# Kernel tuning notes

Measured on AMD Instinct MI355X. Metric: run time of the kernel, lower is better.

Reference implementation:

```python
import jax, jax.numpy as jnp
import numpy as np

B, N, M, C1, C2 = 16, 4096, 1024, 128, 256
MLP0, MLP1 = 256, 256
IN_CH = C1 + C2
EPS = 1e-5


def setup_inputs() -> dict:
    key = jax.random.key(0)
    ks = jax.random.split(key, 6)
    return {
        "xyz1": jax.random.normal(ks[0], (B, 3, N), jnp.float32),
        "xyz2": jax.random.normal(ks[1], (B, 3, M), jnp.float32),
        "points1": jax.random.normal(ks[2], (B, C1, N), jnp.float32),
        "points2": jax.random.normal(ks[3], (B, C2, M), jnp.float32),
        "W1": jax.random.normal(ks[4], (MLP0, IN_CH), jnp.float32) * (1.0 / np.sqrt(IN_CH)),
        "gamma1": jnp.ones((MLP0,), jnp.float32),
        "beta1": jnp.zeros((MLP0,), jnp.float32),
        "W2": jax.random.normal(ks[5], (MLP1, MLP0), jnp.float32) * (1.0 / np.sqrt(MLP0)),
        "gamma2": jnp.ones((MLP1,), jnp.float32),
        "beta2": jnp.zeros((MLP1,), jnp.float32),
    }


def _batchnorm(x, gamma, beta):
    # x: (B, N, C); normalize per channel over batch*length (training-mode BN, biased var)
    mean = jnp.mean(x, axis=(0, 1))
    var = jnp.mean((x - mean) ** 2, axis=(0, 1))
    return (x - mean) * jax.lax.rsqrt(var + EPS) * gamma + beta


def reference(xyz1, xyz2, points1, points2, W1, gamma1, beta1, W2, gamma2, beta2):
    p1 = jnp.swapaxes(xyz1, 1, 2)  # (B, N, 3)
    p2 = jnp.swapaxes(xyz2, 1, 2)  # (B, M, 3)
    # squared pairwise distances (B, N, M); squaring preserves 3-NN ordering,
    # and the original squares the euclidean dist before weighting anyway
    d2 = jnp.sum((p1[:, :, None, :] - p2[:, None, :, :]) ** 2, axis=-1)
    neg_d2, idx = jax.lax.top_k(-d2, 3)  # 3 smallest distances
    dist2 = jnp.maximum(-neg_d2, 1e-10)  # (B, N, 3)
    inv = 1.0 / dist2
    weight = inv / jnp.sum(inv, axis=-1, keepdims=True)  # (B, N, 3)
    f2 = jnp.swapaxes(points2, 1, 2)  # (B, M, C2)
    b, n, k = idx.shape
    gathered = jnp.take_along_axis(
        f2, idx.reshape(b, n * k)[:, :, None], axis=1
    ).reshape(b, n, k, -1)  # (B, N, 3, C2)
    interp = jnp.einsum("bnk,bnkc->bnc", weight, gathered)  # (B, N, C2)
    feat = jnp.concatenate([interp, jnp.swapaxes(points1, 1, 2)], axis=-1)  # (B, N, C1+C2)
    h = jnp.einsum("bnc,oc->bno", feat, W1)  # conv1d k=1, no bias
    h = jax.nn.relu(_batchnorm(h, gamma1, beta1))
    h = jnp.einsum("bnc,oc->bno", h, W2)
    h = jax.nn.relu(_batchnorm(h, gamma2, beta2))
    return jnp.swapaxes(h, 1, 2)  # (B, MLP1, N), channel-first like torch
```

## Files before the change

### kernel.cpp

```cpp
#include <hip/hip_runtime.h>

typedef unsigned short u16;
typedef unsigned int u32;

#define BB 16
#define NN 4096
#define MM 1024
#define C1V 128
#define C2V 256
#define EPSV 1e-5f
#define INV_CNT (1.0f/65536.0f)
#define NREP 32

typedef __attribute__((ext_vector_type(8))) short bf16x8;
typedef __attribute__((ext_vector_type(4))) float f32x4;

static __device__ __forceinline__ u16 f2b(float f) {
  u32 u = __float_as_uint(f);
  u32 r = (u + 0x7FFFu + ((u >> 16) & 1u)) >> 16;
  return (u16)r;
}
static __device__ __forceinline__ float b2f(u16 s) {
  return __uint_as_float(((u32)s) << 16);
}

#define GLD_LDS16(gp, lp)                                                      \
  __builtin_amdgcn_global_load_lds(                                            \
      (const __attribute__((address_space(1))) void*)(gp),                     \
      (__attribute__((address_space(3))) void*)(lp), 16, 0, 0)

__device__ __forceinline__ void tcast_tile64(const float* __restrict__ in,
                                             u16* __restrict__ out, int C,
                                             int P, int p0, int c0, int b,
                                             float (*tile)[33]) {
  int tx = threadIdx.x & 31, ty = threadIdx.x >> 5;
  const float* ib = in + (size_t)b * C * P;
  u16* ob = out + (size_t)b * P * C;
#pragma unroll
  for (int i = 0; i < 8; ++i)
    tile[ty + i * 8][tx] = ib[(size_t)(c0 + ty + i * 8) * P + p0 + tx];
  __syncthreads();
#pragma unroll
  for (int i = 0; i < 4; ++i) {
    int p = ty + i * 8;
    u32 v = (u32)f2b(tile[tx * 2][p]) | ((u32)f2b(tile[tx * 2 + 1][p]) << 16);
    *(u32*)&ob[(size_t)(p0 + p) * C + c0 + tx * 2] = v;
  }
}

__global__ __launch_bounds__(256) void prep_kernel(
    const float* __restrict__ xyz1, const float* __restrict__ xyz2,
    float* __restrict__ pd, int* __restrict__ pi,
    const float* __restrict__ points1, const float* __restrict__ points2,
    u16* __restrict__ p1t, u16* __restrict__ p2t,
    const float* __restrict__ W1, const float* __restrict__ W2,
    u16* __restrict__ W1b, u16* __restrict__ W2b,
    float* __restrict__ statsZero) {
  __shared__ float4 cand[256];
  __shared__ float tile[64][33];
  int bx = blockIdx.x;
  int t = threadIdx.x;

  if (bx < 1024) {
    int c = bx & 3;
    int qt = (bx >> 2) & 15;
    int b = bx >> 6;
    const float* x2b = xyz2 + b * 3 * MM;
    {
      float x = x2b[c * 256 + t];
      float y = x2b[MM + c * 256 + t];
      float z = x2b[2 * MM + c * 256 + t];
      cand[t] = make_float4(x, y, z, x * x + y * y + z * z);
    }
    __syncthreads();
    const float* x1b = xyz1 + b * 3 * NN;
    int n = qt * 256 + t;
    float px = x1b[n], py = x1b[NN + n], pz = x1b[2 * NN + n];
    const float INF = 3.4e38f;
    float k0 = INF, k1 = INF, k2 = INF;
    int j0 = 0, j1 = 0, j2 = 0;
#pragma unroll 8
    for (int m = 0; m < 256; ++m) {
      float4 cd = cand[m];
      float dot = fmaf(px, cd.x, fmaf(py, cd.y, pz * cd.z));
      float key = fmaf(-2.0f, dot, cd.w);
      bool c0 = key < k0, c1 = key < k1, c2 = key < k2;
      k2 = c1 ? k1 : (c2 ? key : k2);
      j2 = c1 ? j1 : (c2 ? m : j2);
      k1 = c0 ? k0 : (c1 ? key : k1);
      j1 = c0 ? j0 : (c1 ? m : j1);
      k0 = c0 ? key : k0;
      j0 = c0 ? m : j0;
    }
    float pn = px * px + py * py + pz * pz;
    int gq = b * NN + n;
    int base = c << 8;
    ((float4*)pd)[(size_t)c * 65536 + gq] =
        make_float4(fmaxf(k0 + pn, 1e-10f), fmaxf(k1 + pn, 1e-10f),
                    fmaxf(k2 + pn, 1e-10f), 0.0f);
    ((int4*)pi)[(size_t)c * 65536 + gq] =
        make_int4(base + j0, base + j1, base + j2, 0);
  } else if (bx < 1664) {
    int i = (bx - 1024) * 256 + t;
    if (i < 98304) W1b[i] = f2b(W1[i]);
    else if (i < 163840) W2b[i - 98304] = f2b(W2[i - 98304]);
  } else if (bx < 1696) {
    ((float4*)statsZero)[(bx - 1664) * 256 + t] =
        make_float4(0.f, 0.f, 0.f, 0.f);
  } else if (bx < 3744) {
    int local = bx - 1696;
    int pt = local & 31, ct = (local >> 5) & 3, b = local >> 7;
    tcast_tile64(points2, p2t, C2V, MM, pt * 32, ct * 64, b, tile);
  } else {
    int local = bx - 3744;
    int pt = local & 127, ct = (local >> 7) & 1, b = local >> 8;
    tcast_tile64(points1, p1t, C1V, NN, pt * 32, ct * 64, b, tile);
  }
}

template <int K, int NTILES, bool OUTB>
__global__ __launch_bounds__(256) void gemm_mfma(
    const u16* __restrict__ A, int lda, const u16* __restrict__ B, int ldb,
    void* __restrict__ out) {
  __shared__ u16 smem[16384];
  int t = threadIdx.x;
  int w = t >> 6, l = t & 63;
  int n0;
  if (NTILES > 0) {
    int p = blockIdx.x;
    int batch = ((p & 7) << 1) | ((p >> 3) & 1);
    int nt = p >> 4;
    n0 = (batch * NTILES + nt) * 128;
  } else {
    n0 = blockIdx.x * 128;
  }
  int o0 = blockIdx.y * 128;

  int wm = w & 1, wn = w >> 1;
  int lr = l >> 2, lc = l & 3;
  int q = l >> 4, m = l & 15;

  f32x4 acc[4][4] = {};
  u16* As = smem;
  u16* Bs = smem + 4096;

  const u16* arow = A + (size_t)n0 * lda;
  const u16* brow = B + (size_t)o0 * ldb;

#pragma unroll
  for (int kt = 0; kt < K; kt += 32) {
    __syncthreads();
#pragma unroll
    for (int r = 0; r < 2; ++r) {
      int row = r * 64 + w * 16 + lr;
      GLD_LDS16(arow + (size_t)row * lda + kt + lc * 8, As + row * 32 + lc * 8);
    }
#pragma unroll
    for (int r = 0; r < 2; ++r) {
      int row = r * 64 + w * 16 + lr;
      GLD_LDS16(brow + (size_t)row * ldb + kt + lc * 8, Bs + row * 32 + lc * 8);
    }
    __syncthreads();
    bf16x8 af[4], bf[4];
#pragma unroll
    for (int i = 0; i < 4; ++i)
      af[i] = *(const bf16x8*)(As + (wm * 64 + i * 16 + m) * 32 + q * 8);
#pragma unroll
    for (int j = 0; j < 4; ++j)
      bf[j] = *(const bf16x8*)(Bs + (wn * 64 + j * 16 + m) * 32 + q * 8);
#pragma unroll
    for (int i = 0; i < 4; ++i)
#pragma unroll
      for (int j = 0; j < 4; ++j)
        acc[i][j] =
            __builtin_amdgcn_mfma_f32_16x16x32_bf16(af[i], bf[j], acc[i][j], 0, 0, 0);
  }

  if (OUTB) {
    __syncthreads();
#pragma unroll
    for (int i = 0; i < 4; ++i)
#pragma unroll
      for (int reg = 0; reg < 4; ++reg) {
        int row = wm * 64 + i * 16 + q * 4 + reg;
#pragma unroll
        for (int j = 0; j < 4; ++j)
          smem[row * 128 + wn * 64 + j * 16 + m] = f2b(acc[i][j][reg]);
      }
    __syncthreads();
    u16* outp = (u16*)out;
    int rbase = w * 32 + (l >> 4);
    int seg = l & 15;
#pragma unroll
    for (int itr = 0; itr < 8; ++itr) {
      int row = rbase + itr * 4;
      uint4 v = *(const uint4*)(smem + row * 128 + seg * 8);
      *(uint4*)(outp + (size_t)(n0 + row) * 256 + o0 + seg * 8) = v;
    }
  } else {
#pragma unroll
    for (int i = 0; i < 4; ++i) {
      int gr = n0 + wm * 64 + i * 16 + q * 4;
#pragma unroll
      for (int reg = 0; reg < 4; ++reg)
#pragma unroll
        for (int j = 0; j < 4; ++j) {
          int gc = o0 + wn * 64 + j * 16 + m;
          ((float*)out)[(size_t)(gr + reg) * 256 + gc] = acc[i][j][reg];
        }
    }
  }
}

__global__ __launch_bounds__(256) void gemm1_32(
    const u16* __restrict__ A, const u16* __restrict__ B,
    u16* __restrict__ out, const u16* __restrict__ G,
    const float* __restrict__ pd, const int* __restrict__ pi,
    float* __restrict__ statsOut) {
  __shared__ __align__(16) u16 smem[9216];
  __shared__ float wsh[32][3];
  __shared__ int ish[32][3];
  int t = threadIdx.x;
  int w = t >> 6, l = t & 63;
  int p = blockIdx.x;
  int batch = ((p & 7) << 1) | ((p >> 3) & 1);
  int nt = p >> 4;
  int n0 = batch * NN + nt * 32;

  if (t < 32) {
    int gq = n0 + t;
    float4 d0 = ((const float4*)pd)[gq];
    int4 ii0 = ((const int4*)pi)[gq];
    float a0 = d0.x, a1 = d0.y, a2 = d0.z;
    int b0 = ii0.x, b1 = ii0.y, b2 = ii0.z;
#pragma unroll
    for (int c = 1; c < 4; ++c) {
      float4 dc = ((const float4*)pd)[(size_t)c * 65536 + gq];
      int4 ic = ((const int4*)pi)[(size_t)c * 65536 + gq];
      float kv[3] = {dc.x, dc.y, dc.z};
      int jv[3] = {ic.x, ic.y, ic.z};
#pragma unroll
      for (int j = 0; j < 3; ++j) {
        float key = kv[j];
        int idx = jv[j];
        bool c0 = key < a0, c1 = key < a1, c2 = key < a2;
        a2 = c1 ? a1 : (c2 ? key : a2);
        b2 = c1 ? b1 : (c2 ? idx : b2);
        a1 = c0 ? a0 : (c1 ? key : a1);
        b1 = c0 ? b0 : (c1 ? idx : b1);
        a0 = c0 ? key : a0;
        b0 = c0 ? idx : b0;
      }
    }
    float v0 = 1.0f / a0, v1 = 1.0f / a1, v2 = 1.0f / a2;
    float s = 1.0f / (v0 + v1 + v2);
    wsh[t][0] = v0 * s; wsh[t][1] = v1 * s; wsh[t][2] = v2 * s;
    ish[t][0] = b0;     ish[t][1] = b1;     ish[t][2] = b2;
  }

  int q = l >> 4, m = l & 15;
  int sr = l >> 2, lc = l & 3;

  f32x4 acc[2][4] = {};
  u16* As = smem;
  u16* Bs = smem + 1024;
  const u16* arow = A + (size_t)n0 * 128;

#pragma unroll
  for (int kt = 0; kt < 128; kt += 32) {
    __syncthreads();
    if (w < 2) {
      int row = w * 16 + sr;
      GLD_LDS16(arow + (size_t)row * 128 + kt + lc * 8, As + row * 32 + lc * 8);
    }
#pragma unroll
    for (int r = 0; r < 4; ++r) {
      int row = r * 64 + w * 16 + sr;
      GLD_LDS16(B + (size_t)row * 384 + kt + lc * 8, Bs + row * 32 + lc * 8);
    }
    __syncthreads();
    bf16x8 af[2], bf[4];
#pragma unroll
    for (int i = 0; i < 2; ++i)
      af[i] = *(const bf16x8*)(As + (i * 16 + m) * 32 + q * 8);
#pragma unroll
    for (int j = 0; j < 4; ++j)
      bf[j] = *(const bf16x8*)(Bs + (w * 64 + j * 16 + m) * 32 + q * 8);
#pragma unroll
    for (int i = 0; i < 2; ++i)
#pragma unroll
      for (int j = 0; j < 4; ++j)
        acc[i][j] =
            __builtin_amdgcn_mfma_f32_16x16x32_bf16(af[i], bf[j], acc[i][j], 0, 0, 0);
  }

  __syncthreads();
  {
    int b = n0 >> 12;
    int rl = t >> 3, oc = t & 7;
    float w0 = wsh[rl][0], w1 = wsh[rl][1], w2 = wsh[rl][2];
    const u16* g0 = G + ((size_t)(b * 1024 + ish[rl][0])) * 256 + oc * 32;
    const u16* g1 = G + ((size_t)(b * 1024 + ish[rl][1])) * 256 + oc * 32;
    const u16* g2 = G + ((size_t)(b * 1024 + ish[rl][2])) * 256 + oc * 32;
    int r3 = rl & 7;
#pragma unroll
    for (int c8 = 0; c8 < 4; ++c8) {
      bf16x8 v0 = *(const bf16x8*)(g0 + c8 * 8);
      bf16x8 v1 = *(const bf16x8*)(g1 + c8 * 8);
      bf16x8 v2 = *(const bf16x8*)(g2 + c8 * 8);
      union { uint4 u; u16 s[8]; } o;
#pragma unroll
      for (int e = 0; e < 8; ++e) {
        float f = w0 * b2f((u16)v0[e]) + w1 * b2f((u16)v1[e]) +
                  w2 * b2f((u16)v2[e]);
        o.s[e] = f2b(f);
      }
      int ch = (oc * 4 + c8) ^ r3;
      *(uint4*)(smem + rl * 256 + ch * 8) = o.u;
    }
  }
  __syncthreads();
#pragma unroll
  for (int i = 0; i < 2; ++i)
#pragma unroll
    for (int reg = 0; reg < 4; ++reg) {
      int row = i * 16 + q * 4 + reg;
      int rx = row & 7;
#pragma unroll
      for (int j = 0; j < 4; ++j) {
        int col = w * 64 + j * 16 + m;
        int off = row * 256 + (((col >> 3) ^ rx) << 3) + (col & 7);
        acc[i][j][reg] += b2f(smem[off]);
      }
    }

  {
    int rep = blockIdx.x & (NREP - 1);
#pragma unroll
    for (int j = 0; j < 4; ++j) {
      float s = 0.0f, ss = 0.0f;
#pragma unroll
      for (int i = 0; i < 2; ++i)
#pragma unroll
        for (int reg = 0; reg < 4; ++reg) {
          float v = acc[i][j][reg];
          s += v;
          ss += v * v;
        }
      s += __shfl_down(s, 32); ss += __shfl_down(ss, 32);
      s += __shfl_down(s, 16); ss += __shfl_down(ss, 16);
      if (l < 16) {
        int c = w * 64 + j * 16 + l;
        atomicAdd(&statsOut[rep * 512 + c], s);
        atomicAdd(&statsOut[rep * 512 + 256 + c], ss);
      }
    }
  }

  __syncthreads();
#pragma unroll
  for (int i = 0; i < 2; ++i)
#pragma unroll
    for (int reg = 0; reg < 4; ++reg) {
      int row = i * 16 + q * 4 + reg;
#pragma unroll
      for (int j = 0; j < 4; ++j)
        smem[row * 256 + w * 64 + j * 16 + m] = f2b(acc[i][j][reg]);
    }
  __syncthreads();
  int rbase = t >> 5, seg = t & 31;
#pragma unroll
  for (int itr = 0; itr < 4; ++itr) {
    int row = rbase + itr * 8;
    uint4 v = *(const uint4*)(smem + row * 256 + seg * 8);
    *(uint4*)(out + (size_t)(n0 + row) * 256 + seg * 8) = v;
  }
}

__global__ __launch_bounds__(256) void gemm2_32(
    const u16* __restrict__ A, const u16* __restrict__ B,
    u16* __restrict__ out, float* __restrict__ statsOut,
    const float* __restrict__ statsInR, const float* __restrict__ gamma,
    const float* __restrict__ beta) {
  __shared__ __align__(16) u16 smem[9216];
  __shared__ float scA[256], shA[256];
  int t = threadIdx.x;
  int w = t >> 6, l = t & 63;
  int n0 = blockIdx.x * 32;

  {
    float s = 0.0f, qq = 0.0f;
#pragma unroll
    for (int r = 0; r < NREP; ++r) {
      s += statsInR[r * 512 + t];
      qq += statsInR[r * 512 + 256 + t];
    }
    float mean = s * INV_CNT;
    float var = qq * INV_CNT - mean * mean;
    float sc = rsqrtf(var + EPSV) * gamma[t];
    scA[t] = sc;
    shA[t] = beta[t] - mean * sc;
  }

  int q = l >> 4, m = l & 15;
  int sr = l >> 2, lc = l & 3;

  f32x4 acc[2][4] = {};
  u16* As = smem;
  u16* Bs = smem + 1024;
  const u16* arow = A + (size_t)n0 * 256;

#pragma unroll
  for (int kt = 0; kt < 256; kt += 32) {
    __syncthreads();
    if (w < 2) {
      int row = w * 16 + sr;
      union { uint4 u; u16 s[8]; } v, o;
      v.u = *(const uint4*)(arow + (size_t)row * 256 + kt + lc * 8);
      int cb = kt + lc * 8;
#pragma unroll
      for (int j = 0; j < 8; ++j) {
        float f = fmaf(b2f(v.s[j]), scA[cb + j], shA[cb + j]);
        o.s[j] = f2b(fmaxf(f, 0.0f));
      }
      *(uint4*)(As + row * 32 + lc * 8) = o.u;
    }
#pragma unroll
    for (int r = 0; r < 4; ++r) {
      int row = r * 64 + w * 16 + sr;
      GLD_LDS16(B + (size_t)row * 256 + kt + lc * 8, Bs + row * 32 + lc * 8);
    }
    __syncthreads();
    bf16x8 af[2], bf[4];
#pragma unroll
    for (int i = 0; i < 2; ++i)
      af[i] = *(const bf16x8*)(As + (i * 16 + m) * 32 + q * 8);
#pragma unroll
    for (int j = 0; j < 4; ++j)
      bf[j] = *(const bf16x8*)(Bs + (w * 64 + j * 16 + m) * 32 + q * 8);
#pragma unroll
    for (int i = 0; i < 2; ++i)
#pragma unroll
      for (int j = 0; j < 4; ++j)
        acc[i][j] =
            __builtin_amdgcn_mfma_f32_16x16x32_bf16(af[i], bf[j], acc[i][j], 0, 0, 0);
  }

  {
    int rep = blockIdx.x & (NREP - 1);
#pragma unroll
    for (int j = 0; j < 4; ++j) {
      float s = 0.0f, ss = 0.0f;
#pragma unroll
      for (int i = 0; i < 2; ++i)
#pragma unroll
        for (int reg = 0; reg < 4; ++reg) {
          float v = acc[i][j][reg];
          s += v;
          ss += v * v;
        }
      s += __shfl_down(s, 32); ss += __shfl_down(ss, 32);
      s += __shfl_down(s, 16); ss += __shfl_down(ss, 16);
      if (l < 16) {
        int c = w * 64 + j * 16 + l;
        atomicAdd(&statsOut[rep * 512 + c], s);
        atomicAdd(&statsOut[rep * 512 + 256 + c], ss);
      }
    }
  }

  __syncthreads();
#pragma unroll
  for (int i = 0; i < 2; ++i)
#pragma unroll
    for (int reg = 0; reg < 4; ++reg) {
      int row = i * 16 + q * 4 + reg;
#pragma unroll
      for (int j = 0; j < 4; ++j)
        smem[row * 256 + w * 64 + j * 16 + m] = f2b(acc[i][j][reg]);
    }
  __syncthreads();
  int rbase = t >> 5, seg = t & 31;
#pragma unroll
  for (int itr = 0; itr < 4; ++itr) {
    int row = rbase + itr * 8;
    uint4 v = *(const uint4*)(smem + row * 256 + seg * 8);
    *(uint4*)(out + (size_t)(n0 + row) * 256 + seg * 8) = v;
  }
}

__global__ __launch_bounds__(256) void bn2t_kernel(
    const u16* __restrict__ h2, const float* __restrict__ statsR,
    const float* __restrict__ gamma, const float* __restrict__ beta,
    float* __restrict__ out) {
  __shared__ float tile[64][65];
  __shared__ float sS[64], sH[64];
  int t = threadIdx.x;
  int n0 = blockIdx.x * 64, c0 = blockIdx.y * 64, b = blockIdx.z;
  if (t < 64) {
    int c = c0 + t;
    float s = 0.0f, qq = 0.0f;
#pragma unroll
    for (int r = 0; r < NREP; ++r) {
      s += statsR[r * 512 + c];
      qq += statsR[r * 512 + 256 + c];
    }
    float mean = s * INV_CNT;
    float var = qq * INV_CNT - mean * mean;
    float sc = rsqrtf(var + EPSV) * gamma[c];
    sS[t] = sc;
    sH[t] = beta[c] - mean * sc;
  }
  __syncthreads();
  int tx = t & 15, ty = t >> 4;
#pragma unroll
  for (int i = 0; i < 4; ++i) {
    int n = ty + i * 16;
    uint2 v = *(const uint2*)(h2 + ((size_t)b * NN + n0 + n) * 256 + c0 + tx * 4);
    int c = tx * 4;
    tile[n][c + 0] = fmaxf(fmaf(b2f((u16)(v.x & 0xffff)), sS[c + 0], sH[c + 0]), 0.0f);
    tile[n][c + 1] = fmaxf(fmaf(b2f((u16)(v.x >> 16)),    sS[c + 1], sH[c + 1]), 0.0f);
    tile[n][c + 2] = fmaxf(fmaf(b2f((u16)(v.y & 0xffff)), sS[c + 2], sH[c + 2]), 0.0f);
    tile[n][c + 3] = fmaxf(fmaf(b2f((u16)(v.y >> 16)),    sS[c + 3], sH[c + 3]), 0.0f);
  }
  __syncthreads();
#pragma unroll
  for (int i = 0; i < 4; ++i) {
    int c = ty + i * 16;
    int nq = tx * 4;
    float4 o4 = make_float4(tile[nq + 0][c], tile[nq + 1][c],
                            tile[nq + 2][c], tile[nq + 3][c]);
    *(float4*)(out + ((size_t)(b * 256 + c0 + c)) * NN + n0 + nq) = o4;
  }
}

extern "C" void kernel_launch(void* const* d_in, const int* in_sizes, int n_in,
                              void* d_out, int out_size, void* d_ws,
                              size_t ws_size, hipStream_t stream) {
  const float* xyz1    = (const float*)d_in[0];
  const float* xyz2    = (const float*)d_in[1];
  const float* points1 = (const float*)d_in[2];
  const float* points2 = (const float*)d_in[3];
  const float* W1      = (const float*)d_in[4];
  const float* gamma1  = (const float*)d_in[5];
  const float* beta1   = (const float*)d_in[6];
  const float* W2      = (const float*)d_in[7];
  const float* gamma2  = (const float*)d_in[8];
  const float* beta2   = (const float*)d_in[9];

  char* ws = (char*)d_ws;
  float* stats1R = (float*)(ws + 0);
  float* stats2R = (float*)(ws + 65536);
  u16*   W1b     = (u16*)(ws + 131072);
  u16*   W2b     = (u16*)(ws + 327680);
  u16*   p2t     = (u16*)(ws + 458752);
  u16*   p1t     = (u16*)(ws + 8847360);
  u16*   G       = (u16*)(ws + 25624576);
  u16*   h2b     = (u16*)(ws + 34013184);
  float* pd      = (float*)(ws + 67567616);
  int*   pi      = (int*)(ws + 71761920);
  u16*   h1b     = (u16*)d_out;
  float* out     = (float*)d_out;

  prep_kernel<<<7840, 256, 0, stream>>>(xyz1, xyz2, pd, pi, points1, points2,
                                        p1t, p2t, W1, W2, W1b, W2b, stats1R);
  gemm_mfma<256, 8, true><<<dim3(128, 2), 256, 0, stream>>>(p2t, 256, W1b, 384,
                                                            G);
  gemm1_32<<<2048, 256, 0, stream>>>(p1t, W1b + 256, h1b, G, pd, pi, stats1R);
  gemm2_32<<<2048, 256, 0, stream>>>(h1b, W2b, h2b, stats2R, stats1R, gamma1,
                                     beta1);
  bn2t_kernel<<<dim3(64, 4, 16), 256, 0, stream>>>(h2b, stats2R, gamma2,
                                                   beta2, out);
}
```

Measured before the change: 222.7 us.

## Interpolate raw features inside GEMM1 instead of precomputing projected G; double-buffer GEMM2

The separate GEMM that projected points2 through the first 256 columns of W1 (G = p2t·W1a) is removed. GEMM1 now builds the interpolated 256-channel feature rows on the fly from p2t, using the 3-NN weights, and runs the full K=384 reduction per 64-row tile. GEMM2 moves to 64-row tiles with double-buffered LDS, so the next A/B slices load while the current MFMAs run. This saves one kernel launch and the G round-trip, but GEMM1 now does 3x more MFMA work and gathers along the K loop with unpipelined global loads.

```diff
diff --git a/kernel.cpp b/kernel.cpp
--- a/kernel.cpp
+++ b/kernel.cpp
@@ -118,116 +118,22 @@
   }
 }
 
-template <int K, int NTILES, bool OUTB>
-__global__ __launch_bounds__(256) void gemm_mfma(
-    const u16* __restrict__ A, int lda, const u16* __restrict__ B, int ldb,
-    void* __restrict__ out) {
-  __shared__ u16 smem[16384];
-  int t = threadIdx.x;
-  int w = t >> 6, l = t & 63;
-  int n0;
-  if (NTILES > 0) {
-    int p = blockIdx.x;
-    int batch = ((p & 7) << 1) | ((p >> 3) & 1);
-    int nt = p >> 4;
-    n0 = (batch * NTILES + nt) * 128;
-  } else {
-    n0 = blockIdx.x * 128;
-  }
-  int o0 = blockIdx.y * 128;
-
-  int wm = w & 1, wn = w >> 1;
-  int lr = l >> 2, lc = l & 3;
-  int q = l >> 4, m = l & 15;
-
-  f32x4 acc[4][4] = {};
-  u16* As = smem;
-  u16* Bs = smem + 4096;
-
-  const u16* arow = A + (size_t)n0 * lda;
-  const u16* brow = B + (size_t)o0 * ldb;
-
-#pragma unroll
-  for (int kt = 0; kt < K; kt += 32) {
-    __syncthreads();
-#pragma unroll
-    for (int r = 0; r < 2; ++r) {
-      int row = r * 64 + w * 16 + lr;
-      GLD_LDS16(arow + (size_t)row * lda + kt + lc * 8, As + row * 32 + lc * 8);
-    }
-#pragma unroll
-    for (int r = 0; r < 2; ++r) {
-      int row = r * 64 + w * 16 + lr;
-      GLD_LDS16(brow + (size_t)row * ldb + kt + lc * 8, Bs + row * 32 + lc * 8);
-    }
-    __syncthreads();
-    bf16x8 af[4], bf[4];
-#pragma unroll
-    for (int i = 0; i < 4; ++i)
-      af[i] = *(const bf16x8*)(As + (wm * 64 + i * 16 + m) * 32 + q * 8);
-#pragma unroll
-    for (int j = 0; j < 4; ++j)
-      bf[j] = *(const bf16x8*)(Bs + (wn * 64 + j * 16 + m) * 32 + q * 8);
-#pragma unroll
-    for (int i = 0; i < 4; ++i)
-#pragma unroll
-      for (int j = 0; j < 4; ++j)
-        acc[i][j] =
-            __builtin_amdgcn_mfma_f32_16x16x32_bf16(af[i], bf[j], acc[i][j], 0, 0, 0);
-  }
-
-  if (OUTB) {
-    __syncthreads();
-#pragma unroll
-    for (int i = 0; i < 4; ++i)
-#pragma unroll
-      for (int reg = 0; reg < 4; ++reg) {
-        int row = wm * 64 + i * 16 + q * 4 + reg;
-#pragma unroll
-        for (int j = 0; j < 4; ++j)
-          smem[row * 128 + wn * 64 + j * 16 + m] = f2b(acc[i][j][reg]);
-      }
-    __syncthreads();
-    u16* outp = (u16*)out;
-    int rbase = w * 32 + (l >> 4);
-    int seg = l & 15;
-#pragma unroll
-    for (int itr = 0; itr < 8; ++itr) {
-      int row = rbase + itr * 4;
-      uint4 v = *(const uint4*)(smem + row * 128 + seg * 8);
-      *(uint4*)(outp + (size_t)(n0 + row) * 256 + o0 + seg * 8) = v;
-    }
-  } else {
-#pragma unroll
-    for (int i = 0; i < 4; ++i) {
-      int gr = n0 + wm * 64 + i * 16 + q * 4;
-#pragma unroll
-      for (int reg = 0; reg < 4; ++reg)
-#pragma unroll
-        for (int j = 0; j < 4; ++j) {
-          int gc = o0 + wn * 64 + j * 16 + m;
-          ((float*)out)[(size_t)(gr + reg) * 256 + gc] = acc[i][j][reg];
-        }
-    }
-  }
-}
-
-__global__ __launch_bounds__(256) void gemm1_32(
-    const u16* __restrict__ A, const u16* __restrict__ B,
-    u16* __restrict__ out, const u16* __restrict__ G,
+__global__ __launch_bounds__(256) void gemm1f(
+    const u16* __restrict__ p1t, const u16* __restrict__ W1b,
+    u16* __restrict__ out, const u16* __restrict__ p2t,
     const float* __restrict__ pd, const int* __restrict__ pi,
     float* __restrict__ statsOut) {
-  __shared__ __align__(16) u16 smem[9216];
-  __shared__ float wsh[32][3];
-  __shared__ int ish[32][3];
+  __shared__ __align__(16) u16 smem[16384];
+  __shared__ float wsh[64][3];
+  __shared__ int ish[64][3];
   int t = threadIdx.x;
   int w = t >> 6, l = t & 63;
   int p = blockIdx.x;
   int batch = ((p & 7) << 1) | ((p >> 3) & 1);
   int nt = p >> 4;
-  int n0 = batch * NN + nt * 32;
-
-  if (t < 32) {
+  int n0 = batch * NN + nt * 64;
+
+  if (t < 64) {
     int gq = n0 + t;
     float4 d0 = ((const float4*)pd)[gq];
     int4 ii0 = ((const int4*)pi)[gq];
@@ -257,90 +163,72 @@
     wsh[t][0] = v0 * s; wsh[t][1] = v1 * s; wsh[t][2] = v2 * s;
     ish[t][0] = b0;     ish[t][1] = b1;     ish[t][2] = b2;
   }
+  __syncthreads();
 
   int q = l >> 4, m = l & 15;
   int sr = l >> 2, lc = l & 3;
-
-  f32x4 acc[2][4] = {};
+  int irow = t >> 2, iseg = t & 3;
+
+  int b = n0 >> 12;
+  float iw0 = wsh[irow][0], iw1 = wsh[irow][1], iw2 = wsh[irow][2];
+  const u16* g0b = p2t + ((size_t)(b * 1024 + ish[irow][0])) * 256 + iseg * 8;
+  const u16* g1b = p2t + ((size_t)(b * 1024 + ish[irow][1])) * 256 + iseg * 8;
+  const u16* g2b = p2t + ((size_t)(b * 1024 + ish[irow][2])) * 256 + iseg * 8;
+
+  f32x4 acc[4][4] = {};
   u16* As = smem;
-  u16* Bs = smem + 1024;
-  const u16* arow = A + (size_t)n0 * 128;
-
-#pragma unroll
-  for (int kt = 0; kt < 128; kt += 32) {
+  u16* Bs = smem + 2048;
+  const u16* arow = p1t + (size_t)n0 * 128;
+
+#pragma unroll
+  for (int kt = 0; kt < 384; kt += 32) {
     __syncthreads();
-    if (w < 2) {
+    if (kt < 256) {
+      bf16x8 v0 = *(const bf16x8*)(g0b + kt);
+      bf16x8 v1 = *(const bf16x8*)(g1b + kt);
+      bf16x8 v2 = *(const bf16x8*)(g2b + kt);
+      union { uint4 u; u16 s[8]; } o;
+#pragma unroll
+      for (int e = 0; e < 8; ++e) {
+        float f = iw0 * b2f((u16)v0[e]) + iw1 * b2f((u16)v1[e]) +
+                  iw2 * b2f((u16)v2[e]);
+        o.s[e] = f2b(f);
+      }
+      *(uint4*)(As + t * 8) = o.u;
+    } else {
       int row = w * 16 + sr;
-      GLD_LDS16(arow + (size_t)row * 128 + kt + lc * 8, As + row * 32 + lc * 8);
+      GLD_LDS16(arow + (size_t)row * 128 + (kt - 256) + lc * 8,
+                As + row * 32 + lc * 8);
     }
 #pragma unroll
     for (int r = 0; r < 4; ++r) {
-      int row = r * 64 + w * 16 + sr;
-      GLD_LDS16(B + (size_t)row * 384 + kt + lc * 8, Bs + row * 32 + lc * 8);
+      int row2 = r * 64 + w * 16 + sr;
+      GLD_LDS16(W1b + (size_t)row2 * 384 + kt + lc * 8,
+                Bs + row2 * 32 + lc * 8);
     }
     __syncthreads();
-    bf16x8 af[2], bf[4];
-#pragma unroll
-    for (int i = 0; i < 2; ++i)
+    bf16x8 af[4], bf[4];
+#pragma unroll
+    for (int i = 0; i < 4; ++i)
       af[i] = *(const bf16x8*)(As + (i * 16 + m) * 32 + q * 8);
 #pragma unroll
     for (int j = 0; j < 4; ++j)
       bf[j] = *(const bf16x8*)(Bs + (w * 64 + j * 16 + m) * 32 + q * 8);
 #pragma unroll
-    for (int i = 0; i < 2; ++i)
+    for (int i = 0; i < 4; ++i)
 #pragma unroll
       for (int j = 0; j < 4; ++j)
         acc[i][j] =
             __builtin_amdgcn_mfma_f32_16x16x32_bf16(af[i], bf[j], acc[i][j], 0, 0, 0);
   }
 
-  __syncthreads();
-  {
-    int b = n0 >> 12;
-    int rl = t >> 3, oc = t & 7;
-    float w0 = wsh[rl][0], w1 = wsh[rl][1], w2 = wsh[rl][2];
-    const u16* g0 = G + ((size_t)(b * 1024 + ish[rl][0])) * 256 + oc * 32;
-    const u16* g1 = G + ((size_t)(b * 1024 + ish[rl][1])) * 256 + oc * 32;
-    const u16* g2 = G + ((size_t)(b * 1024 + ish[rl][2])) * 256 + oc * 32;
-    int r3 = rl & 7;
-#pragma unroll
-    for (int c8 = 0; c8 < 4; ++c8) {
-      bf16x8 v0 = *(const bf16x8*)(g0 + c8 * 8);
-      bf16x8 v1 = *(const bf16x8*)(g1 + c8 * 8);
-      bf16x8 v2 = *(const bf16x8*)(g2 + c8 * 8);
-      union { uint4 u; u16 s[8]; } o;
-#pragma unroll
-      for (int e = 0; e < 8; ++e) {
-        float f = w0 * b2f((u16)v0[e]) + w1 * b2f((u16)v1[e]) +
-                  w2 * b2f((u16)v2[e]);
-        o.s[e] = f2b(f);
-      }
-      int ch = (oc * 4 + c8) ^ r3;
-      *(uint4*)(smem + rl * 256 + ch * 8) = o.u;
-    }
-  }
-  __syncthreads();
-#pragma unroll
-  for (int i = 0; i < 2; ++i)
-#pragma unroll
-    for (int reg = 0; reg < 4; ++reg) {
-      int row = i * 16 + q * 4 + reg;
-      int rx = row & 7;
-#pragma unroll
-      for (int j = 0; j < 4; ++j) {
-        int col = w * 64 + j * 16 + m;
-        int off = row * 256 + (((col >> 3) ^ rx) << 3) + (col & 7);
-        acc[i][j][reg] += b2f(smem[off]);
-      }
-    }
-
   {
     int rep = blockIdx.x & (NREP - 1);
 #pragma unroll
     for (int j = 0; j < 4; ++j) {
       float s = 0.0f, ss = 0.0f;
 #pragma unroll
-      for (int i = 0; i < 2; ++i)
+      for (int i = 0; i < 4; ++i)
 #pragma unroll
         for (int reg = 0; reg < 4; ++reg) {
           float v = acc[i][j][reg];
@@ -359,7 +247,7 @@
 
   __syncthreads();
 #pragma unroll
-  for (int i = 0; i < 2; ++i)
+  for (int i = 0; i < 4; ++i)
 #pragma unroll
     for (int reg = 0; reg < 4; ++reg) {
       int row = i * 16 + q * 4 + reg;
@@ -370,23 +258,23 @@
   __syncthreads();
   int rbase = t >> 5, seg = t & 31;
 #pragma unroll
-  for (int itr = 0; itr < 4; ++itr) {
+  for (int itr = 0; itr < 8; ++itr) {
     int row = rbase + itr * 8;
     uint4 v = *(const uint4*)(smem + row * 256 + seg * 8);
     *(uint4*)(out + (size_t)(n0 + row) * 256 + seg * 8) = v;
   }
 }
 
-__global__ __launch_bounds__(256) void gemm2_32(
+__global__ __launch_bounds__(256) void gemm2_64(
     const u16* __restrict__ A, const u16* __restrict__ B,
     u16* __restrict__ out, float* __restrict__ statsOut,
     const float* __restrict__ statsInR, const float* __restrict__ gamma,
     const float* __restrict__ beta) {
-  __shared__ __align__(16) u16 smem[9216];
+  __shared__ __align__(16) u16 smem[20480];
   __shared__ float scA[256], shA[256];
   int t = threadIdx.x;
   int w = t >> 6, l = t & 63;
-  int n0 = blockIdx.x * 32;
+  int n0 = blockIdx.x * 64;
 
   {
     float s = 0.0f, qq = 0.0f;
@@ -401,49 +289,75 @@
     scA[t] = sc;
     shA[t] = beta[t] - mean * sc;
   }
+  __syncthreads();
 
   int q = l >> 4, m = l & 15;
   int sr = l >> 2, lc = l & 3;
 
-  f32x4 acc[2][4] = {};
-  u16* As = smem;
-  u16* Bs = smem + 1024;
+  f32x4 acc[4][4] = {};
+  u16* Asb[2] = {smem, smem + 2048};
+  u16* Bsb[2] = {smem + 4096, smem + 12288};
   const u16* arow = A + (size_t)n0 * 256;
-
-#pragma unroll
-  for (int kt = 0; kt < 256; kt += 32) {
-    __syncthreads();
-    if (w < 2) {
-      int row = w * 16 + sr;
-      union { uint4 u; u16 s[8]; } v, o;
-      v.u = *(const uint4*)(arow + (size_t)row * 256 + kt + lc * 8);
-      int cb = kt + lc * 8;
-#pragma unroll
-      for (int j = 0; j < 8; ++j) {
-        float f = fmaf(b2f(v.s[j]), scA[cb + j], shA[cb + j]);
-        o.s[j] = f2b(fmaxf(f, 0.0f));
-      }
-      *(uint4*)(As + row * 32 + lc * 8) = o.u;
-    }
+  int arowoff = (w * 16 + sr) * 256 + lc * 8;
+  int aldsoff = (w * 16 + sr) * 32 + lc * 8;
+
+  {
+    union { uint4 u; u16 s[8]; } v, o;
+    v.u = *(const uint4*)(arow + arowoff);
 #pragma unroll
     for (int r = 0; r < 4; ++r) {
-      int row = r * 64 + w * 16 + sr;
-      GLD_LDS16(B + (size_t)row * 256 + kt + lc * 8, Bs + row * 32 + lc * 8);
-    }
-    __syncthreads();
-    bf16x8 af[2], bf[4];
-#pragma unroll
-    for (int i = 0; i < 2; ++i)
-      af[i] = *(const bf16x8*)(As + (i * 16 + m) * 32 + q * 8);
+      int row2 = r * 64 + w * 16 + sr;
+      GLD_LDS16(B + (size_t)row2 * 256 + lc * 8, Bsb[0] + row2 * 32 + lc * 8);
+    }
+    int cb = lc * 8;
+#pragma unroll
+    for (int j = 0; j < 8; ++j) {
+      float f = fmaf(b2f(v.s[j]), scA[cb + j], shA[cb + j]);
+      o.s[j] = f2b(fmaxf(f, 0.0f));
+    }
+    *(uint4*)(Asb[0] + aldsoff) = o.u;
+  }
+  __syncthreads();
+
+#pragma unroll
+  for (int it = 0; it < 8; ++it) {
+    const int cur = it & 1, nxt = cur ^ 1;
+    union { uint4 u; u16 s[8]; } an;
+    if (it < 7) {
+      int kt = (it + 1) * 32;
+      an.u = *(const uint4*)(arow + arowoff + kt);
+#pragma unroll
+      for (int r = 0; r < 4; ++r) {
+        int row2 = r * 64 + w * 16 + sr;
+        GLD_LDS16(B + (size_t)row2 * 256 + kt + lc * 8,
+                  Bsb[nxt] + row2 * 32 + lc * 8);
+      }
+    }
+    bf16x8 af[4], bf[4];
+#pragma unroll
+    for (int i = 0; i < 4; ++i)
+      af[i] = *(const bf16x8*)(Asb[cur] + (i * 16 + m) * 32 + q * 8);
 #pragma unroll
     for (int j = 0; j < 4; ++j)
-      bf[j] = *(const bf16x8*)(Bs + (w * 64 + j * 16 + m) * 32 + q * 8);
-#pragma unroll
-    for (int i = 0; i < 2; ++i)
+      bf[j] = *(const bf16x8*)(Bsb[cur] + (w * 64 + j * 16 + m) * 32 + q * 8);
+#pragma unroll
+    for (int i = 0; i < 4; ++i)
 #pragma unroll
       for (int j = 0; j < 4; ++j)
         acc[i][j] =
             __builtin_amdgcn_mfma_f32_16x16x32_bf16(af[i], bf[j], acc[i][j], 0, 0, 0);
+    if (it < 7) {
+      int kt = (it + 1) * 32;
+      int cb = kt + lc * 8;
+      union { uint4 u; u16 s[8]; } o;
+#pragma unroll
+      for (int j = 0; j < 8; ++j) {
+        float f = fmaf(b2f(an.s[j]), scA[cb + j], shA[cb + j]);
+        o.s[j] = f2b(fmaxf(f, 0.0f));
+      }
+      *(uint4*)(Asb[nxt] + aldsoff) = o.u;
+    }
+    __syncthreads();
   }
 
   {
@@ -452,7 +366,7 @@
     for (int j = 0; j < 4; ++j) {
       float s = 0.0f, ss = 0.0f;
 #pragma unroll
-      for (int i = 0; i < 2; ++i)
+      for (int i = 0; i < 4; ++i)
 #pragma unroll
         for (int reg = 0; reg < 4; ++reg) {
           float v = acc[i][j][reg];
@@ -471,7 +385,7 @@
 
   __syncthreads();
 #pragma unroll
-  for (int i = 0; i < 2; ++i)
+  for (int i = 0; i < 4; ++i)
 #pragma unroll
     for (int reg = 0; reg < 4; ++reg) {
       int row = i * 16 + q * 4 + reg;
@@ -482,7 +396,7 @@
   __syncthreads();
   int rbase = t >> 5, seg = t & 31;
 #pragma unroll
-  for (int itr = 0; itr < 4; ++itr) {
+  for (int itr = 0; itr < 8; ++itr) {
     int row = rbase + itr * 8;
     uint4 v = *(const uint4*)(smem + row * 256 + seg * 8);
     *(uint4*)(out + (size_t)(n0 + row) * 256 + seg * 8) = v;
@@ -555,7 +469,6 @@
   u16*   W2b     = (u16*)(ws + 327680);
   u16*   p2t     = (u16*)(ws + 458752);
   u16*   p1t     = (u16*)(ws + 8847360);
-  u16*   G       = (u16*)(ws + 25624576);
   u16*   h2b     = (u16*)(ws + 34013184);
   float* pd      = (float*)(ws + 67567616);
   int*   pi      = (int*)(ws + 71761920);
@@ -564,10 +477,8 @@
 
   prep_kernel<<<7840, 256, 0, stream>>>(xyz1, xyz2, pd, pi, points1, points2,
                                         p1t, p2t, W1, W2, W1b, W2b, stats1R);
-  gemm_mfma<256, 8, true><<<dim3(128, 2), 256, 0, stream>>>(p2t, 256, W1b, 384,
-                                                            G);
-  gemm1_32<<<2048, 256, 0, stream>>>(p1t, W1b + 256, h1b, G, pd, pi, stats1R);
-  gemm2_32<<<2048, 256, 0, stream>>>(h1b, W2b, h2b, stats2R, stats1R, gamma1,
+  gemm1f<<<1024, 256, 0, stream>>>(p1t, W1b, h1b, p2t, pd, pi, stats1R);
+  gemm2_64<<<1024, 256, 0, stream>>>(h1b, W2b, h2b, stats2R, stats1R, gamma1,
                                      beta1);
   bn2t_kernel<<<dim3(64, 4, 16), 256, 0, stream>>>(h2b, stats2R, gamma2,
                                                    beta2, out);
```

Measured after the change: 209.7 us. 1.06x faster.
